# Optimization experiments

Hardware: AMD Instinct MI355X
Metric: run time of the kernel (lower is better)

## Reference

```python
import jax, jax.numpy as jnp
import numpy as np

H = 16       # num_heads
D = 128      # head_dim
SCALE = 1.0 / np.sqrt(D).astype(np.float32)


def setup_inputs() -> dict:
    key = jax.random.key(0)
    ks = jax.random.split(key, 5)
    B, S, C = 2, 2048, 2048
    x = jax.random.normal(ks[0], (B, S, C), dtype=jnp.float32)
    # nn.Linear stores weight as [out_features, in_features]; scale ~ kaiming-ish
    s = 1.0 / np.sqrt(C)
    wq = jax.random.normal(ks[1], (C, C), dtype=jnp.float32) * s
    wk = jax.random.normal(ks[2], (C, C), dtype=jnp.float32) * s
    wv = jax.random.normal(ks[3], (C, C), dtype=jnp.float32) * s
    wo = jax.random.normal(ks[4], (C, C), dtype=jnp.float32) * s
    return {"x": x, "wq": wq, "wk": wk, "wv": wv, "wo": wo}


def reference(x, wq, wk, wv, wo):
    B, S, C = x.shape
    # projections: nn.Linear(x) = x @ W.T
    q = (x @ wq.T).reshape(B, S, H, D).transpose(0, 2, 1, 3)  # [B,H,S,D]
    k = (x @ wk.T).reshape(B, S, H, D).transpose(0, 2, 1, 3)
    v = (x @ wv.T).reshape(B, S, H, D).transpose(0, 2, 1, 3)
    scores = jnp.einsum('bhqd,bhkd->bhqk', q, k) * SCALE      # [B,H,S,S]
    attn = jax.nn.softmax(scores, axis=-1)
    out = jnp.einsum('bhqk,bhkd->bhqd', attn, v)              # [B,H,S,D]
    out = out.transpose(0, 2, 1, 3).reshape(B, S, H * D)
    return out @ wo.T
```

## Files before the change

### kernel.cpp

```cpp
#include <hip/hip_runtime.h>
#include <hip/hip_bf16.h>
#include <cstdint>
#include <cstddef>

typedef __bf16 bf16_t;
typedef __bf16 bf8_t __attribute__((ext_vector_type(8)));
typedef float f4_t __attribute__((ext_vector_type(4)));
typedef float f8_t __attribute__((ext_vector_type(8)));

#define DEV static __device__ __forceinline__

DEV f4_t mfma16(bf8_t a, bf8_t b, f4_t c) {
    return __builtin_amdgcn_mfma_f32_16x16x32_bf16(a, b, c, 0, 0, 0);
}

DEV bf8_t cvt8(f8_t v) {
    bf8_t r;
#pragma unroll
    for (int i = 0; i < 8; ++i) r[i] = (bf16_t)v[i];
    return r;
}

DEV void load_lds16(const bf16_t* g, bf16_t* l) {
    __builtin_amdgcn_global_load_lds(
        (const __attribute__((address_space(1))) uint32_t*)g,
        (__attribute__((address_space(3))) uint32_t*)l,
        16, 0, 0);
}

__global__ __launch_bounds__(256) void cvt_fused(const float* __restrict__ x,
                                                 const float* __restrict__ wq,
                                                 const float* __restrict__ wk,
                                                 const float* __restrict__ wv,
                                                 bf16_t* __restrict__ xb,
                                                 bf16_t* __restrict__ wqkvb) {
    const int bid = blockIdx.x;
    const float* src;
    bf16_t* dst;
    int base;
    if (bid < 4096) {
        src = x; dst = xb; base = bid;
    } else {
        const int seg = (bid - 4096) >> 11;
        src = (seg == 0) ? wq : (seg == 1) ? wk : wv;
        dst = wqkvb + (size_t)seg * 4194304;
        base = (bid - 4096) & 2047;
    }
    const size_t i = ((size_t)base * 256 + threadIdx.x) * 8;
    const f8_t v = *(const f8_t*)&src[i];
    *(bf8_t*)&dst[i] = cvt8(v);
}

__global__ __launch_bounds__(256) void cvt_bf16(const float* __restrict__ in,
                                                bf16_t* __restrict__ out, int n8) {
    const int i = blockIdx.x * 256 + threadIdx.x;
    if (i < n8) {
        const f8_t v = *(const f8_t*)&in[(size_t)i * 8];
        *(bf8_t*)&out[(size_t)i * 8] = cvt8(v);
    }
}

__global__ __launch_bounds__(512, 2) void gemm_qkv(const bf16_t* __restrict__ A,
                                                   const bf16_t* __restrict__ B,
                                                   bf16_t* __restrict__ Cq,
                                                   bf16_t* __restrict__ Ck,
                                                   bf16_t* __restrict__ Cv) {
    __shared__ bf16_t smem[73728];

    const int tid = threadIdx.x, lane = tid & 63, wave = tid >> 6;
    const int wr = wave >> 2, wc = wave & 3;
    const int q4 = lane >> 4, r16 = lane & 15;
    const int srow = lane >> 2;
    const int scol = ((lane & 3) ^ ((lane >> 3) & 3)) * 8;
    const int rkey = (r16 >> 1) & 3;

    int wg = blockIdx.y * 24 + blockIdx.x;
    wg = (wg & 7) * 96 + (wg >> 3);
    const int bm0 = (wg / 24) * 128;
    const int bn0 = (wg % 24) * 256;

    f4_t acc[4][4] = {};

    auto stageA = [&](int kt, bf16_t* buf) {
#pragma unroll
        for (int kk = 0; kk < 2; ++kk)
            load_lds16(A + (size_t)(bm0 + wave * 16 + srow) * 2048 + kt * 64 + kk * 32 + scol,
                       buf + kk * 4096 + wave * 16 * 32);
    };
    auto stageB = [&](int kt, bf16_t* buf, int rb) {
#pragma unroll
        for (int kk = 0; kk < 2; ++kk)
            load_lds16(B + (size_t)(bn0 + rb + wave * 16 + srow) * 2048 + kt * 64 + kk * 32 + scol,
                       buf + 8192 + kk * 8192 + (rb + wave * 16) * 32);
    };

    {
        stageA(0, smem);
        stageB(0, smem, 0);
        stageB(0, smem, 128);
        stageA(1, smem + 24576);
        stageB(1, smem + 24576, 0);
        stageB(1, smem + 24576, 128);
        asm volatile("s_waitcnt vmcnt(6)" ::: "memory");
        __builtin_amdgcn_s_barrier();
    }

    int cb = 0, sb = 2;
    for (int t = 0; t < 32; ++t) {
        bf16_t* buf  = smem + cb * 24576;
        bf16_t* sbuf = smem + sb * 24576;

        {
            bf8_t af[4], bq[4];
#pragma unroll
            for (int i = 0; i < 4; ++i)
                af[i] = *(const bf8_t*)&buf[(wr * 64 + i * 16 + r16) * 32 + (q4 ^ rkey) * 8];
#pragma unroll
            for (int n = 0; n < 4; ++n)
                bq[n] = *(const bf8_t*)&buf[8192 + (wc * 64 + n * 16 + r16) * 32 +
                                            (q4 ^ rkey) * 8];
            if (t + 2 < 32) {
                stageA(t + 2, sbuf);
                stageB(t + 2, sbuf, 0);
            }
            __builtin_amdgcn_s_barrier();
            asm volatile("s_waitcnt lgkmcnt(0)" ::: "memory");
            __builtin_amdgcn_s_setprio(1);
#pragma unroll
            for (int i = 0; i < 4; ++i)
#pragma unroll
                for (int n = 0; n < 4; ++n)
                    acc[i][n] = mfma16(af[i], bq[n], acc[i][n]);
            __builtin_amdgcn_s_setprio(0);
            __builtin_amdgcn_s_barrier();
        }

        {
            bf8_t af[4], bq[4];
#pragma unroll
            for (int i = 0; i < 4; ++i)
                af[i] = *(const bf8_t*)&buf[4096 + (wr * 64 + i * 16 + r16) * 32 +
                                            (q4 ^ rkey) * 8];
#pragma unroll
            for (int n = 0; n < 4; ++n)
                bq[n] = *(const bf8_t*)&buf[8192 + 8192 + (wc * 64 + n * 16 + r16) * 32 +
                                            (q4 ^ rkey) * 8];
            if (t + 2 < 32)
                stageB(t + 2, sbuf, 128);
            __builtin_amdgcn_s_barrier();
            asm volatile("s_waitcnt lgkmcnt(0)" ::: "memory");
            __builtin_amdgcn_s_setprio(1);
#pragma unroll
            for (int i = 0; i < 4; ++i)
#pragma unroll
                for (int n = 0; n < 4; ++n)
                    acc[i][n] = mfma16(af[i], bq[n], acc[i][n]);
            __builtin_amdgcn_s_setprio(0);
            if (t < 30) {
                asm volatile("s_waitcnt vmcnt(6)" ::: "memory");
            } else {
                asm volatile("s_waitcnt vmcnt(0)" ::: "memory");
            }
            __builtin_amdgcn_s_barrier();
        }

        cb = (cb == 2) ? 0 : cb + 1;
        sb = (sb == 2) ? 0 : sb + 1;
    }

    __syncthreads();

    bf16_t* strip = smem + wave * 4608;
    if (bn0 < 4096) {
        bf16_t* dst = (bn0 < 2048) ? Cq : Ck;
        const int nb = (bn0 & 2047) + wc * 64;
#pragma unroll
        for (int i = 0; i < 4; ++i)
#pragma unroll
            for (int n = 0; n < 4; ++n)
#pragma unroll
                for (int r = 0; r < 4; ++r)
                    strip[(i * 16 + q4 * 4 + r) * 72 + n * 16 + r16] =
                        (bf16_t)acc[i][n][r];
        asm volatile("s_waitcnt lgkmcnt(0)" ::: "memory");
#pragma unroll
        for (int it = 0; it < 8; ++it) {
            const int row = it * 8 + (lane >> 3);
            const int c = (lane & 7) * 8;
            *(bf8_t*)&dst[(size_t)(bm0 + wr * 64 + row) * 2048 + nb + c] =
                *(const bf8_t*)&strip[row * 72 + c];
        }
    } else {
        const int bb = bm0 >> 11;
        const int s0 = (bm0 & 2047) + wr * 64;
#pragma unroll
        for (int i = 0; i < 4; ++i)
#pragma unroll
            for (int n = 0; n < 4; ++n)
#pragma unroll
                for (int r = 0; r < 4; ++r)
                    strip[(n * 16 + r16) * 72 + i * 16 + q4 * 4 + r] =
                        (bf16_t)acc[i][n][r];
        asm volatile("s_waitcnt lgkmcnt(0)" ::: "memory");
#pragma unroll
        for (int it = 0; it < 8; ++it) {
            const int nrow = it * 8 + (lane >> 3);
            const int c = (lane & 7) * 8;
            const int dg = (bn0 - 4096) + wc * 64 + nrow;
            const int h = dg >> 7, d = dg & 127;
            *(bf8_t*)&Cv[(((size_t)(bb * 16 + h) * 128 + d) << 11) + s0 + c] =
                *(const bf8_t*)&strip[nrow * 72 + c];
        }
    }
}

__global__ __launch_bounds__(512, 2) void gemm_out(const bf16_t* __restrict__ A,
                                                   const bf16_t* __restrict__ B,
                                                   float* __restrict__ C) {
    __shared__ bf16_t smem[73728];

    const int tid = threadIdx.x, lane = tid & 63, wave = tid >> 6;
    const int wr = wave >> 2, wc = wave & 3;
    const int q4 = lane >> 4, r16 = lane & 15;
    const int srow = lane >> 2;
    const int scol = ((lane & 3) ^ ((lane >> 3) & 3)) * 8;
    const int rkey = (r16 >> 1) & 3;

    int wg = blockIdx.y * 8 + blockIdx.x;
    wg = (wg & 7) * 32 + (wg >> 3);
    const int bm0 = (wg / 8) * 128;
    const int bn0 = (wg % 8) * 256;

    f4_t acc[4][4] = {};

    auto stageA = [&](int kt, bf16_t* buf) {
#pragma unroll
        for (int kk = 0; kk < 2; ++kk)
            load_lds16(A + (size_t)(bm0 + wave * 16 + srow) * 2048 + kt * 64 + kk * 32 + scol,
                       buf + kk * 4096 + wave * 16 * 32);
    };
    auto stageB = [&](int kt, bf16_t* buf, int rb) {
#pragma unroll
        for (int kk = 0; kk < 2; ++kk)
            load_lds16(B + (size_t)(bn0 + rb + wave * 16 + srow) * 2048 + kt * 64 + kk * 32 + scol,
                       buf + 8192 + kk * 8192 + (rb + wave * 16) * 32);
    };

    {
        stageA(0, smem);
        stageB(0, smem, 0);
        stageB(0, smem, 128);
        stageA(1, smem + 24576);
        stageB(1, smem + 24576, 0);
        stageB(1, smem + 24576, 128);
        asm volatile("s_waitcnt vmcnt(6)" ::: "memory");
        __builtin_amdgcn_s_barrier();
    }

    int cb = 0, sb = 2;
    for (int t = 0; t < 32; ++t) {
        bf16_t* buf  = smem + cb * 24576;
        bf16_t* sbuf = smem + sb * 24576;

        {
            bf8_t af[4], bq[4];
#pragma unroll
            for (int i = 0; i < 4; ++i)
                af[i] = *(const bf8_t*)&buf[(wr * 64 + i * 16 + r16) * 32 + (q4 ^ rkey) * 8];
#pragma unroll
            for (int n = 0; n < 4; ++n)
                bq[n] = *(const bf8_t*)&buf[8192 + (wc * 64 + n * 16 + r16) * 32 +
                                            (q4 ^ rkey) * 8];
            if (t + 2 < 32) {
                stageA(t + 2, sbuf);
                stageB(t + 2, sbuf, 0);
            }
            __builtin_amdgcn_s_barrier();
            asm volatile("s_waitcnt lgkmcnt(0)" ::: "memory");
            __builtin_amdgcn_s_setprio(1);
#pragma unroll
            for (int i = 0; i < 4; ++i)
#pragma unroll
                for (int n = 0; n < 4; ++n)
                    acc[i][n] = mfma16(af[i], bq[n], acc[i][n]);
            __builtin_amdgcn_s_setprio(0);
            __builtin_amdgcn_s_barrier();
        }

        {
            bf8_t af[4], bq[4];
#pragma unroll
            for (int i = 0; i < 4; ++i)
                af[i] = *(const bf8_t*)&buf[4096 + (wr * 64 + i * 16 + r16) * 32 +
                                            (q4 ^ rkey) * 8];
#pragma unroll
            for (int n = 0; n < 4; ++n)
                bq[n] = *(const bf8_t*)&buf[8192 + 8192 + (wc * 64 + n * 16 + r16) * 32 +
                                            (q4 ^ rkey) * 8];
            if (t + 2 < 32)
                stageB(t + 2, sbuf, 128);
            __builtin_amdgcn_s_barrier();
            asm volatile("s_waitcnt lgkmcnt(0)" ::: "memory");
            __builtin_amdgcn_s_setprio(1);
#pragma unroll
            for (int i = 0; i < 4; ++i)
#pragma unroll
                for (int n = 0; n < 4; ++n)
                    acc[i][n] = mfma16(af[i], bq[n], acc[i][n]);
            __builtin_amdgcn_s_setprio(0);
            if (t < 30) {
                asm volatile("s_waitcnt vmcnt(6)" ::: "memory");
            } else {
                asm volatile("s_waitcnt vmcnt(0)" ::: "memory");
            }
            __builtin_amdgcn_s_barrier();
        }

        cb = (cb == 2) ? 0 : cb + 1;
        sb = (sb == 2) ? 0 : sb + 1;
    }

#pragma unroll
    for (int i = 0; i < 4; ++i)
#pragma unroll
        for (int n = 0; n < 4; ++n)
#pragma unroll
            for (int r = 0; r < 4; ++r) {
                const int m = bm0 + wr * 64 + i * 16 + q4 * 4 + r;
                const int nn = bn0 + wc * 64 + n * 16 + r16;
                C[(size_t)m * 2048 + nn] = acc[i][n][r];
            }
}

__global__ __launch_bounds__(256) void flash5(const bf16_t* __restrict__ Q,
                                              const bf16_t* __restrict__ K,
                                              const bf16_t* __restrict__ VT,
                                              bf16_t* __restrict__ O) {
    constexpr int S = 2048, C = 2048;
    constexpr float SCL = 0.08838834764831845f * 1.4426950408889634f;
    __shared__ bf16_t Ks[4 * 64 * 32];
    __shared__ bf16_t Vs[2 * 128 * 32];
    __shared__ bf16_t Ps[4][32 * 72];

    const int tid = threadIdx.x, lane = tid & 63, wave = tid >> 6;
    const int q4 = lane >> 4, r16 = lane & 15;
    const int bh = blockIdx.y, b = bh >> 4, h = bh & 15;
    const int q0 = blockIdx.x * 128 + wave * 32;

    const size_t qrow = (size_t)b * S + q0;
    const bf16_t* Qp0 = Q + (qrow + r16) * C + h * 128;
    const bf16_t* Qp1 = Q + (qrow + 16 + r16) * C + h * 128;
    const bf16_t* Kbase = K + (size_t)b * S * C + h * 128;
    const bf16_t* Vbase = VT + (size_t)bh * 128 * S;
    bf16_t* Pw = &Ps[wave][0];

    const int srow = lane >> 2;
    const int scol = (((lane & 3) ^ ((lane >> 3) & 3))) * 8;
    const int rkey = (r16 >> 1) & 3;

    bf8_t aq0[4], aq1[4];
#pragma unroll
    for (int kk = 0; kk < 4; ++kk) {
        aq0[kk] = *(const bf8_t*)&Qp0[kk * 32 + q4 * 8];
        aq1[kk] = *(const bf8_t*)&Qp1[kk * 32 + q4 * 8];
    }

    bf8_t ones;
#pragma unroll
    for (int i = 0; i < 8; ++i) ones[i] = (bf16_t)1.0f;

    f4_t o0[8] = {}, o1[8] = {};
    f4_t lacc0 = {}, lacc1 = {};

    for (int kv0 = 0; kv0 < S; kv0 += 64) {
        __syncthreads();
#pragma unroll
        for (int r0 = 0; r0 < 64; r0 += 16)
            load_lds16(Kbase + (size_t)(kv0 + r0 + srow) * C + wave * 32 + scol,
                       Ks + wave * 2048 + r0 * 32);
        {
            const int kkp = wave >> 1;
            const int rb = (wave & 1) * 64;
#pragma unroll
            for (int r0 = 0; r0 < 64; r0 += 16)
                load_lds16(Vbase + (size_t)(rb + r0 + srow) * S + kv0 + kkp * 32 + scol,
                           Vs + kkp * 4096 + (rb + r0) * 32);
        }
        __syncthreads();

        f4_t s4a[4] = {}, s4b[4] = {};
#pragma unroll
        for (int kk = 0; kk < 4; ++kk) {
#pragma unroll
            for (int j = 0; j < 4; ++j) {
                const bf8_t bk =
                    *(const bf8_t*)&Ks[kk * 2048 + (j * 16 + r16) * 32 + (q4 ^ rkey) * 8];
                s4a[j] = mfma16(aq0[kk], bk, s4a[j]);
                s4b[j] = mfma16(aq1[kk], bk, s4b[j]);
            }
        }

#pragma unroll
        for (int r = 0; r < 4; ++r)
#pragma unroll
            for (int j = 0; j < 4; ++j) {
                Pw[(q4 * 4 + r) * 72 + j * 16 + r16] = (bf16_t)exp2f(s4a[j][r] * SCL);
                Pw[(16 + q4 * 4 + r) * 72 + j * 16 + r16] = (bf16_t)exp2f(s4b[j][r] * SCL);
            }
        asm volatile("s_waitcnt lgkmcnt(0)" ::: "memory");

        bf8_t ap0[2], ap1[2];
#pragma unroll
        for (int kkp = 0; kkp < 2; ++kkp) {
            ap0[kkp] = *(const bf8_t*)&Pw[r16 * 72 + kkp * 32 + q4 * 8];
            ap1[kkp] = *(const bf8_t*)&Pw[(16 + r16) * 72 + kkp * 32 + q4 * 8];
        }

#pragma unroll
        for (int kkp = 0; kkp < 2; ++kkp) {
            lacc0 = mfma16(ap0[kkp], ones, lacc0);
            lacc1 = mfma16(ap1[kkp], ones, lacc1);
        }

#pragma unroll
        for (int t = 0; t < 8; ++t) {
#pragma unroll
            for (int kkp = 0; kkp < 2; ++kkp) {
                const bf8_t bv =
                    *(const bf8_t*)&Vs[kkp * 4096 + (t * 16 + r16) * 32 + (q4 ^ rkey) * 8];
                o0[t] = mfma16(ap0[kkp], bv, o0[t]);
                o1[t] = mfma16(ap1[kkp], bv, o1[t]);
            }
        }
    }

    f4_t inv0, inv1;
#pragma unroll
    for (int r = 0; r < 4; ++r) {
        inv0[r] = 1.0f / lacc0[r];
        inv1[r] = 1.0f / lacc1[r];
    }
#pragma unroll
    for (int t = 0; t < 8; ++t)
#pragma unroll
        for (int r = 0; r < 4; ++r) {
            O[(qrow + q4 * 4 + r) * C + h * 128 + t * 16 + r16] = (bf16_t)(o0[t][r] * inv0[r]);
            O[(qrow + 16 + q4 * 4 + r) * C + h * 128 + t * 16 + r16] =
                (bf16_t)(o1[t][r] * inv1[r]);
        }
}

extern "C" void kernel_launch(void* const* d_in, const int* in_sizes, int n_in,
                              void* d_out, int out_size, void* d_ws, size_t ws_size,
                              hipStream_t stream) {
    const float* x  = (const float*)d_in[0];
    const float* wq = (const float*)d_in[1];
    const float* wk = (const float*)d_in[2];
    const float* wv = (const float*)d_in[3];
    const float* wo = (const float*)d_in[4];

    bf16_t* ws = (bf16_t*)d_ws;
    bf16_t* xb   = ws;
    bf16_t* Wqkv = ws + 8388608;
    bf16_t* Qb   = ws + 20971520;
    bf16_t* Kb   = ws + 29360128;
    bf16_t* Vt   = ws + 37748736;
    bf16_t* Wob  = xb;
    bf16_t* At   = Wqkv;

    cvt_fused<<<10240, 256, 0, stream>>>(x, wq, wk, wv, xb, Wqkv);

    gemm_qkv<<<dim3(24, 32), 512, 0, stream>>>(xb, Wqkv, Qb, Kb, Vt);

    cvt_bf16<<<2048, 256, 0, stream>>>(wo, Wob, 524288);

    flash5<<<dim3(16, 32), 256, 0, stream>>>(Qb, Kb, Vt, At);

    gemm_out<<<dim3(8, 32), 512, 0, stream>>>(At, Wob, (float*)d_out);
}
```

Before: 392.8 us.

## Split QKV GEMM into 256x256-tile QK kernel and separate V kernel

Splits the fused QKV projection GEMM into two kernels. The Q/K part uses larger 256x256 output tiles with a double-buffered LDS pipeline, giving each wave 8x4 accumulators. The V part keeps the old 128x256 tiling with its transposed epilogue. The aim is higher arithmetic intensity and fewer blocks for the bulk of the projection work. The cost is an extra launch, more register pressure, and only 256 blocks for the QK GEMM, which may leave CUs underutilised.

```diff
diff --git a/kernel.cpp b/kernel.cpp
--- a/kernel.cpp
+++ b/kernel.cpp
@@ -60,12 +60,19 @@
     }
 }
 
-__global__ __launch_bounds__(512, 2) void gemm_qkv(const bf16_t* __restrict__ A,
-                                                   const bf16_t* __restrict__ B,
-                                                   bf16_t* __restrict__ Cq,
-                                                   bf16_t* __restrict__ Ck,
-                                                   bf16_t* __restrict__ Cv) {
-    __shared__ bf16_t smem[73728];
+DEV void stage_half(const bf16_t* X, int row0, int rb, int kt, bf16_t* bufX,
+                    int wave, int srow, int scol) {
+#pragma unroll
+    for (int kk = 0; kk < 2; ++kk)
+        load_lds16(X + (size_t)(row0 + rb + wave * 16 + srow) * 2048 + kt * 64 + kk * 32 + scol,
+                   bufX + kk * 8192 + (rb + wave * 16) * 32);
+}
+
+__global__ __launch_bounds__(512, 2) void gemm_qk(const bf16_t* __restrict__ A,
+                                                  const bf16_t* __restrict__ B,
+                                                  bf16_t* __restrict__ Cq,
+                                                  bf16_t* __restrict__ Ck) {
+    __shared__ bf16_t smem[65536];
 
     const int tid = threadIdx.x, lane = tid & 63, wave = tid >> 6;
     const int wr = wave >> 2, wc = wave & 3;
@@ -74,10 +81,125 @@
     const int scol = ((lane & 3) ^ ((lane >> 3) & 3)) * 8;
     const int rkey = (r16 >> 1) & 3;
 
-    int wg = blockIdx.y * 24 + blockIdx.x;
-    wg = (wg & 7) * 96 + (wg >> 3);
-    const int bm0 = (wg / 24) * 128;
-    const int bn0 = (wg % 24) * 256;
+    int wg = blockIdx.y * 16 + blockIdx.x;
+    wg = (wg & 7) * 32 + (wg >> 3);
+    const int bm0 = (wg / 16) * 256;
+    const int bn0 = (wg % 16) * 256;
+
+    f4_t acc[8][4] = {};
+
+    {
+        bf16_t* b0 = smem;
+        bf16_t* b1 = smem + 32768;
+        stage_half(A, bm0, 0,   0, b0,          wave, srow, scol);
+        stage_half(A, bm0, 128, 0, b0,          wave, srow, scol);
+        stage_half(B, bn0, 0,   0, b0 + 16384,  wave, srow, scol);
+        stage_half(B, bn0, 128, 0, b0 + 16384,  wave, srow, scol);
+        stage_half(B, bn0, 0,   1, b1 + 16384,  wave, srow, scol);
+        stage_half(B, bn0, 128, 1, b1 + 16384,  wave, srow, scol);
+        asm volatile("s_waitcnt vmcnt(4)" ::: "memory");
+        __builtin_amdgcn_s_barrier();
+    }
+
+    for (int t = 0; t < 32; ++t) {
+        bf16_t* buf  = smem + (t & 1) * 32768;
+        bf16_t* bufN = smem + ((t + 1) & 1) * 32768;
+
+        bf8_t bq[4][2];
+#pragma unroll
+        for (int p = 0; p < 4; ++p) {
+            if (p == 0) {
+#pragma unroll
+                for (int n = 0; n < 4; ++n)
+#pragma unroll
+                    for (int kk = 0; kk < 2; ++kk)
+                        bq[n][kk] = *(const bf8_t*)&buf[16384 + kk * 8192 +
+                                                       (wc * 64 + n * 16 + r16) * 32 +
+                                                       (q4 ^ rkey) * 8];
+            }
+            bf8_t af[2][2];
+#pragma unroll
+            for (int i = 0; i < 2; ++i)
+#pragma unroll
+                for (int kk = 0; kk < 2; ++kk)
+                    af[i][kk] = *(const bf8_t*)&buf[kk * 8192 +
+                                                    (wr * 128 + (2 * p + i) * 16 + r16) * 32 +
+                                                    (q4 ^ rkey) * 8];
+
+            if (p == 0 && t + 1 < 32) {
+                stage_half(A, bm0, 0,   t + 1, bufN, wave, srow, scol);
+                stage_half(A, bm0, 128, t + 1, bufN, wave, srow, scol);
+            }
+            if (p == 1 && t + 2 < 32)
+                stage_half(B, bn0, 0,   t + 2, buf + 16384, wave, srow, scol);
+            if (p == 2 && t + 2 < 32)
+                stage_half(B, bn0, 128, t + 2, buf + 16384, wave, srow, scol);
+
+            __builtin_amdgcn_s_barrier();
+            asm volatile("s_waitcnt lgkmcnt(0)" ::: "memory");
+            __builtin_amdgcn_s_setprio(1);
+#pragma unroll
+            for (int kk = 0; kk < 2; ++kk)
+#pragma unroll
+                for (int i = 0; i < 2; ++i)
+#pragma unroll
+                    for (int n = 0; n < 4; ++n)
+                        acc[2 * p + i][n] = mfma16(af[i][kk], bq[n][kk], acc[2 * p + i][n]);
+            __builtin_amdgcn_s_setprio(0);
+            if (p == 3) {
+                if (t < 30) {
+                    asm volatile("s_waitcnt vmcnt(4)" ::: "memory");
+                } else {
+                    asm volatile("s_waitcnt vmcnt(0)" ::: "memory");
+                }
+            }
+            __builtin_amdgcn_s_barrier();
+        }
+    }
+
+    __syncthreads();
+
+    bf16_t* strip = smem + wave * 4608;
+    bf16_t* dst = (bn0 < 2048) ? Cq : Ck;
+    const int nb = (bn0 & 2047) + wc * 64;
+#pragma unroll
+    for (int P = 0; P < 2; ++P) {
+#pragma unroll
+        for (int i = 0; i < 4; ++i)
+#pragma unroll
+            for (int n = 0; n < 4; ++n)
+#pragma unroll
+                for (int r = 0; r < 4; ++r)
+                    strip[(i * 16 + q4 * 4 + r) * 72 + n * 16 + r16] =
+                        (bf16_t)acc[P * 4 + i][n][r];
+        asm volatile("s_waitcnt lgkmcnt(0)" ::: "memory");
+#pragma unroll
+        for (int it = 0; it < 8; ++it) {
+            const int row = it * 8 + (lane >> 3);
+            const int c = (lane & 7) * 8;
+            *(bf8_t*)&dst[(size_t)(bm0 + wr * 128 + P * 64 + row) * 2048 + nb + c] =
+                *(const bf8_t*)&strip[row * 72 + c];
+        }
+        asm volatile("s_waitcnt lgkmcnt(0)" ::: "memory");
+    }
+}
+
+__global__ __launch_bounds__(512, 2) void gemm_v(const bf16_t* __restrict__ A,
+                                                 const bf16_t* __restrict__ B,
+                                                 bf16_t* __restrict__ Cv) {
+    __shared__ bf16_t smem[73728];
+
+    const int tid = threadIdx.x, lane = tid & 63, wave = tid >> 6;
+    const int wr = wave >> 2, wc = wave & 3;
+    const int q4 = lane >> 4, r16 = lane & 15;
+    const int srow = lane >> 2;
+    const int scol = ((lane & 3) ^ ((lane >> 3) & 3)) * 8;
+    const int rkey = (r16 >> 1) & 3;
+
+    int wg = blockIdx.y * 8 + blockIdx.x;
+    wg = (wg & 7) * 32 + (wg >> 3);
+    const int bm0 = (wg / 8) * 128;
+    const int bn0 = (wg % 8) * 256;
 
     f4_t acc[4][4] = {};
 
@@ -171,46 +293,25 @@
     __syncthreads();
 
     bf16_t* strip = smem + wave * 4608;
-    if (bn0 < 4096) {
-        bf16_t* dst = (bn0 < 2048) ? Cq : Ck;
-        const int nb = (bn0 & 2047) + wc * 64;
-#pragma unroll
-        for (int i = 0; i < 4; ++i)
-#pragma unroll
-            for (int n = 0; n < 4; ++n)
-#pragma unroll
-                for (int r = 0; r < 4; ++r)
-                    strip[(i * 16 + q4 * 4 + r) * 72 + n * 16 + r16] =
-                        (bf16_t)acc[i][n][r];
-        asm volatile("s_waitcnt lgkmcnt(0)" ::: "memory");
-#pragma unroll
-        for (int it = 0; it < 8; ++it) {
-            const int row = it * 8 + (lane >> 3);
-            const int c = (lane & 7) * 8;
-            *(bf8_t*)&dst[(size_t)(bm0 + wr * 64 + row) * 2048 + nb + c] =
-                *(const bf8_t*)&strip[row * 72 + c];
-        }
-    } else {
-        const int bb = bm0 >> 11;
-        const int s0 = (bm0 & 2047) + wr * 64;
-#pragma unroll
-        for (int i = 0; i < 4; ++i)
-#pragma unroll
-            for (int n = 0; n < 4; ++n)
-#pragma unroll
-                for (int r = 0; r < 4; ++r)
-                    strip[(n * 16 + r16) * 72 + i * 16 + q4 * 4 + r] =
-                        (bf16_t)acc[i][n][r];
-        asm volatile("s_waitcnt lgkmcnt(0)" ::: "memory");
-#pragma unroll
-        for (int it = 0; it < 8; ++it) {
-            const int nrow = it * 8 + (lane >> 3);
-            const int c = (lane & 7) * 8;
-            const int dg = (bn0 - 4096) + wc * 64 + nrow;
-            const int h = dg >> 7, d = dg & 127;
-            *(bf8_t*)&Cv[(((size_t)(bb * 16 + h) * 128 + d) << 11) + s0 + c] =
-                *(const bf8_t*)&strip[nrow * 72 + c];
-        }
+    const int bb = bm0 >> 11;
+    const int s0 = (bm0 & 2047) + wr * 64;
+#pragma unroll
+    for (int i = 0; i < 4; ++i)
+#pragma unroll
+        for (int n = 0; n < 4; ++n)
+#pragma unroll
+            for (int r = 0; r < 4; ++r)
+                strip[(n * 16 + r16) * 72 + i * 16 + q4 * 4 + r] =
+                    (bf16_t)acc[i][n][r];
+    asm volatile("s_waitcnt lgkmcnt(0)" ::: "memory");
+#pragma unroll
+    for (int it = 0; it < 8; ++it) {
+        const int nrow = it * 8 + (lane >> 3);
+        const int c = (lane & 7) * 8;
+        const int dg = bn0 + wc * 64 + nrow;
+        const int h = dg >> 7, d = dg & 127;
+        *(bf8_t*)&Cv[(((size_t)(bb * 16 + h) * 128 + d) << 11) + s0 + c] =
+            *(const bf8_t*)&strip[nrow * 72 + c];
     }
 }
 
@@ -470,7 +571,9 @@
 
     cvt_fused<<<10240, 256, 0, stream>>>(x, wq, wk, wv, xb, Wqkv);
 
-    gemm_qkv<<<dim3(24, 32), 512, 0, stream>>>(xb, Wqkv, Qb, Kb, Vt);
+    gemm_qk<<<dim3(16, 16), 512, 0, stream>>>(xb, Wqkv, Qb, Kb);
+
+    gemm_v<<<dim3(8, 32), 512, 0, stream>>>(xb, Wqkv + 8388608, Vt);
 
     cvt_bf16<<<2048, 256, 0, stream>>>(wo, Wob, 524288);
 
```

Result: faster. 371.0 us (-5.5%).
